# Kernel optimization log

Hardware: AMD Instinct MI355X
Metric: run time of the kernel (lower is better)

## Reference

```python
import jax, jax.numpy as jnp
import numpy as np

C = 512        # channels
CTX = 768      # context_dim


def setup_inputs() -> dict:
    key = jax.random.key(0)
    ks = jax.random.split(key, 10)
    B, H, W = 8, 64, 64
    Lc = 512
    s = 0.02
    return {
        "x": jax.random.normal(ks[0], (B, C, H, W), jnp.float32),
        "context": jax.random.normal(ks[1], (B, Lc, CTX), jnp.float32),
        "Wq": jax.random.normal(ks[2], (C, C), jnp.float32) * s,
        "bq": jnp.zeros((C,), jnp.float32),
        "Wk": jax.random.normal(ks[3], (CTX, C), jnp.float32) * s,
        "bk": jnp.zeros((C,), jnp.float32),
        "Wv": jax.random.normal(ks[4], (CTX, C), jnp.float32) * s,
        "bv": jnp.zeros((C,), jnp.float32),
        "Wo": jax.random.normal(ks[5], (C, C), jnp.float32) * s,
        "bo": jnp.zeros((C,), jnp.float32),
    }


def reference(x, context, Wq, bq, Wk, bk, Wv, bv, Wo, bo):
    B, Cdim, H, W = x.shape
    scale = Cdim ** (-0.5)
    # [B, HW, C]
    xr = x.reshape(B, Cdim, H * W).transpose(0, 2, 1)
    q = xr @ Wq + bq                      # [B, HW, C]
    k = context @ Wk + bk                 # [B, Lc, C]
    v = context @ Wv + bv                 # [B, Lc, C]
    sim = jnp.einsum('bqc,bkc->bqk', q, k) * scale
    attn = jax.nn.softmax(sim, axis=-1)
    out = jnp.einsum('bqk,bkc->bqc', attn, v)
    out = out @ Wo + bo                   # [B, HW, C]
    out = out.transpose(0, 2, 1).reshape(B, Cdim, H, W)
    return x + out
```

## Files before the change

kernel.cpp:

```cpp
#include <hip/hip_runtime.h>
#include <hip/hip_bf16.h>

typedef __bf16 bf16_t;
typedef bf16_t bf16x8 __attribute__((ext_vector_type(8)));
typedef bf16_t bf16x4 __attribute__((ext_vector_type(4)));
typedef float  f32x4  __attribute__((ext_vector_type(4)));

constexpr int B_ = 8, C_ = 512, HW_ = 4096, LC_ = 512, CTX_ = 768;


__global__ void k_transpose_w(const float* __restrict__ in, bf16_t* __restrict__ out,
                              int R, int Cc) {
    __shared__ float t[32][33];
    int r0 = blockIdx.x * 32, c0 = blockIdx.y * 32;
    int tx = threadIdx.x, ty = threadIdx.y;
#pragma unroll
    for (int i = 0; i < 4; ++i)
        t[ty + i * 8][tx] = in[(size_t)(r0 + ty + i * 8) * Cc + c0 + tx];
    __syncthreads();
#pragma unroll
    for (int i = 0; i < 4; ++i)
        out[(size_t)(c0 + ty + i * 8) * R + r0 + tx] = (bf16_t)t[tx][ty + i * 8];
}

__global__ void k_bias(const float* __restrict__ bk, const float* __restrict__ bv,
                       const bf16_t* __restrict__ Wo_t, const float* __restrict__ bo,
                       float* __restrict__ bkvo) {
    int blk = blockIdx.x, tid = threadIdx.x;
    if (blk >= 128) {
        int i = (blk - 128) * 256 + tid;
        bkvo[i] = bk[i];
        return;
    }
    int wave = tid >> 6, lane = tid & 63;
    int cc = blk * 4 + wave;
    bf16x8 w = *(const bf16x8*)&Wo_t[(size_t)cc * C_ + lane * 8];
    float s = 0.f;
#pragma unroll
    for (int j = 0; j < 8; ++j) s += bv[lane * 8 + j] * (float)w[j];
#pragma unroll
    for (int o = 32; o > 0; o >>= 1) s += __shfl_xor(s, o);
    if (lane == 0) bkvo[512 + cc] = s + bo[cc];
}

__global__ void k_f32_to_bf16(const float* __restrict__ in, bf16_t* __restrict__ out, int n) {
    int i = (blockIdx.x * 256 + threadIdx.x) * 4;
    if (i >= n) return;
    f32x4 v = *(const f32x4*)(in + i);
    bf16x4 w;
    w[0] = (bf16_t)v.x; w[1] = (bf16_t)v.y; w[2] = (bf16_t)v.z; w[3] = (bf16_t)v.w;
    *(bf16x4*)(out + i) = w;
}

template <int MODE>
__global__ __launch_bounds__(256) void k_gemm(
    const bf16_t* __restrict__ A, int lda, long sA,
    const bf16_t* __restrict__ Bt, int ldb, long sB,
    const float* __restrict__ bias,
    void* __restrict__ out_, long sOut,
    int N, int K, float scale) {
    __shared__ bf16_t lA[128 * 32];
    __shared__ bf16_t lB[128 * 32];
    const int z = blockIdx.z;
    A  += (size_t)z * sA;
    Bt += (size_t)z * sB;
    const int tid  = threadIdx.x;
    const int lane = tid & 63;
    const int wave = tid >> 6;
    const int wm = (wave >> 1) * 64, wn = (wave & 1) * 64;
    const int bm0 = blockIdx.y * 128, bn0 = blockIdx.x * 128;
    const int ar = lane & 15, kc = lane >> 4;

    auto lA3 = (__attribute__((address_space(3))) char*)&lA[0];
    auto lB3 = (__attribute__((address_space(3))) char*)&lB[0];

    f32x4 acc[4][4] = {};

    for (int k0 = 0; k0 < K; k0 += 32) {
        __syncthreads();
#pragma unroll
        for (int s = 0; s < 2; ++s) {
            int wchunk = wave * 2 + s;
            int id = wchunk * 64 + lane;
            int row = id >> 2, c4 = id & 3;
            __builtin_amdgcn_global_load_lds(
                (const __attribute__((address_space(1))) void*)
                    &A[(size_t)(bm0 + row) * lda + k0 + c4 * 8],
                (__attribute__((address_space(3))) void*)(lA3 + wchunk * 1024),
                16, 0, 0);
            __builtin_amdgcn_global_load_lds(
                (const __attribute__((address_space(1))) void*)
                    &Bt[(size_t)(bn0 + row) * ldb + k0 + c4 * 8],
                (__attribute__((address_space(3))) void*)(lB3 + wchunk * 1024),
                16, 0, 0);
        }
        __syncthreads();
        bf16x8 af[4], bfr[4];
#pragma unroll
        for (int f = 0; f < 4; ++f) {
            af[f]  = *(const bf16x8*)&lA[(wm + f * 16 + ar) * 32 + kc * 8];
            bfr[f] = *(const bf16x8*)&lB[(wn + f * 16 + ar) * 32 + kc * 8];
        }
#pragma unroll
        for (int fm = 0; fm < 4; ++fm)
#pragma unroll
            for (int fn = 0; fn < 4; ++fn)
                acc[fm][fn] = __builtin_amdgcn_mfma_f32_16x16x32_bf16(
                    af[fm], bfr[fn], acc[fm][fn], 0, 0, 0);
    }

    const int rj = (lane >> 4) * 4;
    const int cj = lane & 15;

#pragma unroll
    for (int fm = 0; fm < 4; ++fm) {
#pragma unroll
        for (int fn = 0; fn < 4; ++fn) {
            int r0 = bm0 + wm + fm * 16 + rj;
            int cc = bn0 + wn + fn * 16 + cj;
            if constexpr (MODE == 3) {
                bf16_t* out = (bf16_t*)out_;
                bf16x4 v;
#pragma unroll
                for (int j = 0; j < 4; ++j) v[j] = (bf16_t)acc[fm][fn][j];
                *(bf16x4*)&out[(size_t)cc * sOut + r0] = v;
            } else {
                float bb = bias[cc];
                if (cc < 512) {
                    bf16_t* o = (bf16_t*)out_;
#pragma unroll
                    for (int j = 0; j < 4; ++j)
                        o[(size_t)(r0 + j) * 512 + cc] = (bf16_t)(acc[fm][fn][j] + bb);
                } else {
                    bf16_t* o = (bf16_t*)out_ + (size_t)B_ * LC_ * C_;
                    int b = r0 >> 9, l0 = r0 & 511;
                    bf16x4 v;
#pragma unroll
                    for (int j = 0; j < 4; ++j) v[j] = (bf16_t)(acc[fm][fn][j] + bb);
                    *(bf16x4*)&o[((size_t)b * C_ + (cc - 512)) * LC_ + l0] = v;
                }
            }
        }
    }
}

__global__ __launch_bounds__(512, 2) void k_flash(
    const bf16_t* __restrict__ Wq_t, const float* __restrict__ bq,
    const bf16_t* __restrict__ Kb, const bf16_t* __restrict__ Vt,
    const float* __restrict__ x, float* __restrict__ out) {
    __shared__ bf16_t lQP[64 * 512];
    __shared__ bf16_t lS[3][16384];
    float (*redA)[64] = (float(*)[64])&lQP[0];
    float (*redB)[64] = (float(*)[64])&lQP[512];

    const int bid = blockIdx.x;
    const int z = bid & 7;
    const int q0 = (bid >> 3) * 64;
    const int tid = threadIdx.x;
    const int lane = tid & 63;
    const int wave = tid >> 6;
    const int wm2 = wave >> 2;
    const int wn4 = wave & 3;
    const int h = lane >> 4;
    const int r15 = lane & 15;

    const bf16_t* Kz = Kb + (size_t)z * LC_ * C_;
    const bf16_t* Vz = Vt + (size_t)z * C_ * LC_;
    const float*  xz = x + (size_t)z * C_ * HW_;

    auto lS3 = (__attribute__((address_space(3))) char*)&lS[0][0];

    auto STAGE = [&](int b, const bf16_t* __restrict__ src, int t) {
#pragma unroll
        for (int s = 0; s < 4; ++s) {
            int id = s * 512 + tid;
            int row = id >> 2, c4 = id & 3;
            int c4s = c4 ^ (row & 3);
            __builtin_amdgcn_global_load_lds(
                (const __attribute__((address_space(1))) void*)
                    &src[(size_t)row * 512 + t * 32 + c4s * 8],
                (__attribute__((address_space(3))) void*)
                    (lS3 + b * 32768 + s * 8192 + wave * 1024),
                16, 0, 0);
        }
    };

    f32x4 acc[2][8];
    bf16x8 af0[2], bf0[8], af1[2], bf1[8];

    auto READF = [&](bf16x8 (&af)[2], bf16x8 (&bfr)[8], int t, int buf) {
        int c16 = t * 4 + h;
#pragma unroll
        for (int m = 0; m < 2; ++m) {
            int row = wm2 * 32 + m * 16 + r15;
            int sc = (c16 & 56) | ((c16 ^ row) & 7);
            af[m] = *(const bf16x8*)&lQP[row * 512 + sc * 8];
        }
        const bf16_t* lb = &lS[buf][0];
#pragma unroll
        for (int n = 0; n < 8; ++n) {
            int row = wn4 * 128 + n * 16 + r15;
            bfr[n] = *(const bf16x8*)&lb[row * 32 + (h ^ (row & 3)) * 8];
        }
    };
    auto MF = [&](bf16x8 (&af)[2], bf16x8 (&bfr)[8]) {
        __builtin_amdgcn_s_setprio(1);
#pragma unroll
        for (int m = 0; m < 2; ++m)
#pragma unroll
            for (int n = 0; n < 8; ++n)
                acc[m][n] = __builtin_amdgcn_mfma_f32_16x16x32_bf16(
                    af[m], bfr[n], acc[m][n], 0, 0, 0);
        __builtin_amdgcn_s_setprio(0);
    };
    auto BAR = [&]() {
        __builtin_amdgcn_sched_barrier(0);
        __builtin_amdgcn_s_barrier();
        __builtin_amdgcn_sched_barrier(0);
    };

    auto PHASE = [&](const bf16_t* __restrict__ src, int off) {
        READF(af0, bf0, 0, off % 3);
#pragma unroll
        for (int tt = 0; tt < 7; ++tt) {
            int t = 2 * tt;
            STAGE((t + 2 + off) % 3, src, t + 2);
            MF(af0, bf0);
            asm volatile("s_waitcnt vmcnt(4)" ::: "memory");
            READF(af1, bf1, t + 1, (t + 1 + off) % 3);
            BAR();
            STAGE((t + 3 + off) % 3, src, t + 3);
            MF(af1, bf1);
            asm volatile("s_waitcnt vmcnt(4)" ::: "memory");
            READF(af0, bf0, t + 2, (t + 2 + off) % 3);
            BAR();
        }
        MF(af0, bf0);
        asm volatile("s_waitcnt vmcnt(0)" ::: "memory");
        READF(af1, bf1, 15, (15 + off) % 3);
        BAR();
        MF(af1, bf1);
    };

    STAGE(0, Wq_t, 0); STAGE(1, Wq_t, 1);
#pragma unroll
    for (int i = 0; i < 16; ++i) {
        int c = i * 32 + (tid >> 4);
        int q = (tid & 15) * 4;
        f32x4 v = *(const f32x4*)&xz[(size_t)c * HW_ + q0 + q];
#pragma unroll
        for (int j = 0; j < 4; ++j) {
            int row = q + j;
            int c16 = c >> 3;
            int sc = (c16 & 56) | ((c16 ^ row) & 7);
            lQP[row * 512 + sc * 8 + (c & 7)] = (bf16_t)v[j];
        }
    }
    __syncthreads();

#pragma unroll
    for (int m = 0; m < 2; ++m)
#pragma unroll
        for (int n = 0; n < 8; ++n) acc[m][n] = (f32x4)0.f;
    PHASE(Wq_t, 0);

    __syncthreads();
    STAGE(1, Kz, 0); STAGE(2, Kz, 1);
    {
        float bqv[8];
#pragma unroll
        for (int n = 0; n < 8; ++n) bqv[n] = bq[wn4 * 128 + n * 16 + r15];
#pragma unroll
        for (int m = 0; m < 2; ++m)
#pragma unroll
            for (int j = 0; j < 4; ++j) {
                int row = wm2 * 32 + m * 16 + h * 4 + j;
#pragma unroll
                for (int n = 0; n < 8; ++n) {
                    int col = wn4 * 128 + n * 16 + r15;
                    int c16 = col >> 3;
                    int sc = (c16 & 56) | ((c16 ^ row) & 7);
                    lQP[row * 512 + sc * 8 + (col & 7)] = (bf16_t)(acc[m][n][j] + bqv[n]);
                }
            }
    }
    __syncthreads();

#pragma unroll
    for (int m = 0; m < 2; ++m)
#pragma unroll
        for (int n = 0; n < 8; ++n) acc[m][n] = (f32x4)0.f;
    PHASE(Kz, 1);

    __syncthreads();
    STAGE(2, Vz, 0); STAGE(0, Vz, 1);
    const float scale = 0.044194173824159216f;
    float M[2][4], inv[2][4];
#pragma unroll
    for (int m = 0; m < 2; ++m)
#pragma unroll
        for (int j = 0; j < 4; ++j) {
            float v = -1e30f;
#pragma unroll
            for (int n = 0; n < 8; ++n) v = fmaxf(v, acc[m][n][j]);
#pragma unroll
            for (int o = 1; o < 16; o <<= 1) v = fmaxf(v, __shfl_xor(v, o));
            if (r15 == 0) redA[wn4][wm2 * 32 + m * 16 + h * 4 + j] = v;
        }
    __syncthreads();
#pragma unroll
    for (int m = 0; m < 2; ++m)
#pragma unroll
        for (int j = 0; j < 4; ++j) {
            int row = wm2 * 32 + m * 16 + h * 4 + j;
            M[m][j] = fmaxf(fmaxf(redA[0][row], redA[1][row]),
                            fmaxf(redA[2][row], redA[3][row]));
        }
#pragma unroll
    for (int m = 0; m < 2; ++m)
#pragma unroll
        for (int j = 0; j < 4; ++j) {
            float s = 0.f;
#pragma unroll
            for (int n = 0; n < 8; ++n) {
                float e = __expf((acc[m][n][j] - M[m][j]) * scale);
                acc[m][n][j] = e;
                s += e;
            }
#pragma unroll
            for (int o = 1; o < 16; o <<= 1) s += __shfl_xor(s, o);
            if (r15 == 0) redB[wn4][wm2 * 32 + m * 16 + h * 4 + j] = s;
        }
    __syncthreads();
#pragma unroll
    for (int m = 0; m < 2; ++m)
#pragma unroll
        for (int j = 0; j < 4; ++j) {
            int row = wm2 * 32 + m * 16 + h * 4 + j;
            inv[m][j] = 1.f / (redB[0][row] + redB[1][row] +
                               redB[2][row] + redB[3][row]);
        }
    __syncthreads();
#pragma unroll
    for (int m = 0; m < 2; ++m)
#pragma unroll
        for (int j = 0; j < 4; ++j) {
            int row = wm2 * 32 + m * 16 + h * 4 + j;
#pragma unroll
            for (int n = 0; n < 8; ++n) {
                int col = wn4 * 128 + n * 16 + r15;
                int c16 = col >> 3;
                int sc = (c16 & 56) | ((c16 ^ row) & 7);
                lQP[row * 512 + sc * 8 + (col & 7)] = (bf16_t)(acc[m][n][j] * inv[m][j]);
            }
        }
    __syncthreads();

#pragma unroll
    for (int m = 0; m < 2; ++m)
#pragma unroll
        for (int n = 0; n < 8; ++n) acc[m][n] = (f32x4)0.f;
    PHASE(Vz, 2);

    float* oz = out + (size_t)z * C_ * HW_;
#pragma unroll
    for (int m = 0; m < 2; ++m)
#pragma unroll
        for (int n = 0; n < 8; ++n) {
            int r0 = q0 + wm2 * 32 + m * 16 + h * 4;
            int cc = wn4 * 128 + n * 16 + r15;
            f32x4 xv = *(const f32x4*)&xz[(size_t)cc * HW_ + r0];
            f32x4 o;
#pragma unroll
            for (int j = 0; j < 4; ++j) o[j] = acc[m][n][j] + xv[j];
            *(f32x4*)&oz[(size_t)cc * HW_ + r0] = o;
        }
}

extern "C" void kernel_launch(void* const* d_in, const int* in_sizes, int n_in,
                              void* d_out, int out_size, void* d_ws, size_t ws_size,
                              hipStream_t stream) {
    (void)in_sizes; (void)n_in; (void)out_size; (void)ws_size;
    const float* x   = (const float*)d_in[0];
    const float* ctx = (const float*)d_in[1];
    const float* Wq  = (const float*)d_in[2];
    const float* bq  = (const float*)d_in[3];
    const float* Wk  = (const float*)d_in[4];
    const float* bk  = (const float*)d_in[5];
    const float* Wv  = (const float*)d_in[6];
    const float* bv  = (const float*)d_in[7];
    const float* Wo  = (const float*)d_in[8];
    const float* bo  = (const float*)d_in[9];
    float* out = (float*)d_out;

    char* ws = (char*)d_ws;
    size_t off = 0;
    auto alloc = [&](size_t bytes) {
        char* p = ws + off;
        off += (bytes + 255) & ~(size_t)255;
        return p;
    };
    bf16_t* Wq_t  = (bf16_t*)alloc((size_t)C_ * C_ * 2);
    bf16_t* Wk_t  = (bf16_t*)alloc((size_t)C_ * CTX_ * 2);
    bf16_t* Wvo_t = (bf16_t*)alloc((size_t)C_ * CTX_ * 2);
    bf16_t* Wv_b  = (bf16_t*)alloc((size_t)CTX_ * C_ * 2);
    bf16_t* Wo_t  = (bf16_t*)alloc((size_t)C_ * C_ * 2);
    float*  bkvo  = (float*)alloc((size_t)1024 * 4);
    bf16_t* ctxb  = (bf16_t*)alloc((size_t)B_ * LC_ * CTX_ * 2);
    bf16_t* Kb    = (bf16_t*)alloc((size_t)B_ * LC_ * C_ * 2);
    bf16_t* Vt    = (bf16_t*)alloc((size_t)B_ * C_ * LC_ * 2);

    k_transpose_w<<<dim3(C_ / 32, C_ / 32), dim3(32, 8), 0, stream>>>(Wq, Wq_t, C_, C_);
    k_transpose_w<<<dim3(CTX_ / 32, C_ / 32), dim3(32, 8), 0, stream>>>(Wk, Wk_t, CTX_, C_);
    k_transpose_w<<<dim3(C_ / 32, C_ / 32), dim3(32, 8), 0, stream>>>(Wo, Wo_t, C_, C_);
    k_f32_to_bf16<<<(CTX_ * C_ / 4 + 255) / 256, 256, 0, stream>>>(Wv, Wv_b, CTX_ * C_);
    k_bias<<<130, 256, 0, stream>>>(bk, bv, Wo_t, bo, bkvo);
    k_f32_to_bf16<<<(B_ * LC_ * CTX_ / 4 + 255) / 256, 256, 0, stream>>>(
        ctx, ctxb, B_ * LC_ * CTX_);

    k_gemm<3><<<dim3(4, 6, 1), 256, 0, stream>>>(
        Wv_b, C_, 0, Wo_t, C_, 0, nullptr, Wvo_t, CTX_, C_, C_, 1.f);
    k_gemm<4><<<dim3(8, 32, 1), 256, 0, stream>>>(
        ctxb, CTX_, 0, Wk_t, CTX_, 0, bkvo, Kb, 0, 1024, CTX_, 1.f);
    k_flash<<<512, 512, 0, stream>>>(Wq_t, bq, Kb, Vt, x, out);
}
```

Before: 165.6 us.

## Change LDS swizzles, simplify flash pipeline loop, merge weight transposes

Changes the LDS swizzle for the Q/P tile (adds row>>3 into the XOR) and for the staged K/V/W tiles (uses row>>1) to reduce bank conflicts on the fragment reads. It replaces the double-buffered register prefetch in the phase loop with a simpler per-iteration load-then-compute loop, which lowers register pressure but exposes LDS read latency. It also merges three weight-transpose launches into one kernel using blockIdx.z, and moves redB to avoid overlap with redA.

Measured after the change: 188.6 us. +13.8%, slower.

```diff
diff --git a/kernel.cpp b/kernel.cpp
--- a/kernel.cpp
+++ b/kernel.cpp
@@ -9,14 +9,21 @@
 constexpr int B_ = 8, C_ = 512, HW_ = 4096, LC_ = 512, CTX_ = 768;
 
 
-__global__ void k_transpose_w(const float* __restrict__ in, bf16_t* __restrict__ out,
-                              int R, int Cc) {
+__global__ void k_transpose_w3(const float* __restrict__ Wq, const float* __restrict__ Wk,
+                               const float* __restrict__ Wo,
+                               bf16_t* __restrict__ Wq_t, bf16_t* __restrict__ Wk_t,
+                               bf16_t* __restrict__ Wo_t) {
     __shared__ float t[32][33];
+    int zz = blockIdx.z;
+    const float* in = (zz == 0) ? Wq : (zz == 1) ? Wk : Wo;
+    bf16_t* out     = (zz == 0) ? Wq_t : (zz == 1) ? Wk_t : Wo_t;
+    int R = (zz == 1) ? CTX_ : C_;
     int r0 = blockIdx.x * 32, c0 = blockIdx.y * 32;
+    if (r0 >= R) return;
     int tx = threadIdx.x, ty = threadIdx.y;
 #pragma unroll
     for (int i = 0; i < 4; ++i)
-        t[ty + i * 8][tx] = in[(size_t)(r0 + ty + i * 8) * Cc + c0 + tx];
+        t[ty + i * 8][tx] = in[(size_t)(r0 + ty + i * 8) * C_ + c0 + tx];
     __syncthreads();
 #pragma unroll
     for (int i = 0; i < 4; ++i)
@@ -144,6 +151,7 @@
     }
 }
 
+#define SWZ(c16, row) ((((c16)) & 56) | (((c16) ^ (row) ^ ((row) >> 3)) & 7))
 __global__ __launch_bounds__(512, 2) void k_flash(
     const bf16_t* __restrict__ Wq_t, const float* __restrict__ bq,
     const bf16_t* __restrict__ Kb, const bf16_t* __restrict__ Vt,
@@ -151,7 +159,7 @@
     __shared__ bf16_t lQP[64 * 512];
     __shared__ bf16_t lS[3][16384];
     float (*redA)[64] = (float(*)[64])&lQP[0];
-    float (*redB)[64] = (float(*)[64])&lQP[512];
+    float (*redB)[64] = (float(*)[64])&lQP[1024];
 
     const int bid = blockIdx.x;
     const int z = bid & 7;
@@ -175,7 +183,7 @@
         for (int s = 0; s < 4; ++s) {
             int id = s * 512 + tid;
             int row = id >> 2, c4 = id & 3;
-            int c4s = c4 ^ (row & 3);
+            int c4s = c4 ^ ((row >> 1) & 3);
             __builtin_amdgcn_global_load_lds(
                 (const __attribute__((address_space(1))) void*)
                     &src[(size_t)row * 512 + t * 32 + c4s * 8],
@@ -186,60 +194,39 @@
     };
 
     f32x4 acc[2][8];
-    bf16x8 af0[2], bf0[8], af1[2], bf1[8];
-
-    auto READF = [&](bf16x8 (&af)[2], bf16x8 (&bfr)[8], int t, int buf) {
-        int c16 = t * 4 + h;
-#pragma unroll
-        for (int m = 0; m < 2; ++m) {
-            int row = wm2 * 32 + m * 16 + r15;
-            int sc = (c16 & 56) | ((c16 ^ row) & 7);
-            af[m] = *(const bf16x8*)&lQP[row * 512 + sc * 8];
-        }
-        const bf16_t* lb = &lS[buf][0];
-#pragma unroll
-        for (int n = 0; n < 8; ++n) {
-            int row = wn4 * 128 + n * 16 + r15;
-            bfr[n] = *(const bf16x8*)&lb[row * 32 + (h ^ (row & 3)) * 8];
-        }
-    };
-    auto MF = [&](bf16x8 (&af)[2], bf16x8 (&bfr)[8]) {
-        __builtin_amdgcn_s_setprio(1);
-#pragma unroll
-        for (int m = 0; m < 2; ++m)
-#pragma unroll
-            for (int n = 0; n < 8; ++n)
-                acc[m][n] = __builtin_amdgcn_mfma_f32_16x16x32_bf16(
-                    af[m], bfr[n], acc[m][n], 0, 0, 0);
-        __builtin_amdgcn_s_setprio(0);
-    };
-    auto BAR = [&]() {
-        __builtin_amdgcn_sched_barrier(0);
-        __builtin_amdgcn_s_barrier();
-        __builtin_amdgcn_sched_barrier(0);
-    };
 
     auto PHASE = [&](const bf16_t* __restrict__ src, int off) {
-        READF(af0, bf0, 0, off % 3);
-#pragma unroll
-        for (int tt = 0; tt < 7; ++tt) {
-            int t = 2 * tt;
-            STAGE((t + 2 + off) % 3, src, t + 2);
-            MF(af0, bf0);
-            asm volatile("s_waitcnt vmcnt(4)" ::: "memory");
-            READF(af1, bf1, t + 1, (t + 1 + off) % 3);
-            BAR();
-            STAGE((t + 3 + off) % 3, src, t + 3);
-            MF(af1, bf1);
-            asm volatile("s_waitcnt vmcnt(4)" ::: "memory");
-            READF(af0, bf0, t + 2, (t + 2 + off) % 3);
-            BAR();
-        }
-        MF(af0, bf0);
-        asm volatile("s_waitcnt vmcnt(0)" ::: "memory");
-        READF(af1, bf1, 15, (15 + off) % 3);
-        BAR();
-        MF(af1, bf1);
+        for (int t = 0; t < 16; ++t) {
+            if (t <= 13) STAGE((t + 2 + off) % 3, src, t + 2);
+            bf16x8 af[2], bfr[8];
+            int c16 = t * 4 + h;
+#pragma unroll
+            for (int m = 0; m < 2; ++m) {
+                int row = wm2 * 32 + m * 16 + r15;
+                af[m] = *(const bf16x8*)&lQP[row * 512 + SWZ(c16, row) * 8];
+            }
+            const bf16_t* lb = &lS[(t + off) % 3][0];
+#pragma unroll
+            for (int n = 0; n < 8; ++n) {
+                int row = wn4 * 128 + n * 16 + r15;
+                bfr[n] = *(const bf16x8*)&lb[row * 32 + ((h ^ (row >> 1)) & 3) * 8];
+            }
+            __builtin_amdgcn_s_setprio(1);
+#pragma unroll
+            for (int m = 0; m < 2; ++m)
+#pragma unroll
+                for (int n = 0; n < 8; ++n)
+                    acc[m][n] = __builtin_amdgcn_mfma_f32_16x16x32_bf16(
+                        af[m], bfr[n], acc[m][n], 0, 0, 0);
+            __builtin_amdgcn_s_setprio(0);
+            if (t < 15) {
+                if (t <= 13) asm volatile("s_waitcnt vmcnt(4)" ::: "memory");
+                else         asm volatile("s_waitcnt vmcnt(0)" ::: "memory");
+                __builtin_amdgcn_sched_barrier(0);
+                __builtin_amdgcn_s_barrier();
+                __builtin_amdgcn_sched_barrier(0);
+            }
+        }
     };
 
     STAGE(0, Wq_t, 0); STAGE(1, Wq_t, 1);
@@ -248,12 +235,11 @@
         int c = i * 32 + (tid >> 4);
         int q = (tid & 15) * 4;
         f32x4 v = *(const f32x4*)&xz[(size_t)c * HW_ + q0 + q];
+        int c16 = c >> 3;
 #pragma unroll
         for (int j = 0; j < 4; ++j) {
             int row = q + j;
-            int c16 = c >> 3;
-            int sc = (c16 & 56) | ((c16 ^ row) & 7);
-            lQP[row * 512 + sc * 8 + (c & 7)] = (bf16_t)v[j];
+            lQP[row * 512 + SWZ(c16, row) * 8 + (c & 7)] = (bf16_t)v[j];
         }
     }
     __syncthreads();
@@ -279,8 +265,8 @@
                 for (int n = 0; n < 8; ++n) {
                     int col = wn4 * 128 + n * 16 + r15;
                     int c16 = col >> 3;
-                    int sc = (c16 & 56) | ((c16 ^ row) & 7);
-                    lQP[row * 512 + sc * 8 + (col & 7)] = (bf16_t)(acc[m][n][j] + bqv[n]);
+                    lQP[row * 512 + SWZ(c16, row) * 8 + (col & 7)] =
+                        (bf16_t)(acc[m][n][j] + bqv[n]);
                 }
             }
     }
@@ -350,8 +336,8 @@
             for (int n = 0; n < 8; ++n) {
                 int col = wn4 * 128 + n * 16 + r15;
                 int c16 = col >> 3;
-                int sc = (c16 & 56) | ((c16 ^ row) & 7);
-                lQP[row * 512 + sc * 8 + (col & 7)] = (bf16_t)(acc[m][n][j] * inv[m][j]);
+                lQP[row * 512 + SWZ(c16, row) * 8 + (col & 7)] =
+                    (bf16_t)(acc[m][n][j] * inv[m][j]);
             }
         }
     __syncthreads();
@@ -410,9 +396,8 @@
     bf16_t* Kb    = (bf16_t*)alloc((size_t)B_ * LC_ * C_ * 2);
     bf16_t* Vt    = (bf16_t*)alloc((size_t)B_ * C_ * LC_ * 2);
 
-    k_transpose_w<<<dim3(C_ / 32, C_ / 32), dim3(32, 8), 0, stream>>>(Wq, Wq_t, C_, C_);
-    k_transpose_w<<<dim3(CTX_ / 32, C_ / 32), dim3(32, 8), 0, stream>>>(Wk, Wk_t, CTX_, C_);
-    k_transpose_w<<<dim3(C_ / 32, C_ / 32), dim3(32, 8), 0, stream>>>(Wo, Wo_t, C_, C_);
+    k_transpose_w3<<<dim3(CTX_ / 32, C_ / 32, 3), dim3(32, 8), 0, stream>>>(
+        Wq, Wk, Wo, Wq_t, Wk_t, Wo_t);
     k_f32_to_bf16<<<(CTX_ * C_ / 4 + 255) / 256, 256, 0, stream>>>(Wv, Wv_b, CTX_ * C_);
     k_bias<<<130, 256, 0, stream>>>(bk, bv, Wo_t, bo, bkvo);
     k_f32_to_bf16<<<(B_ * LC_ * CTX_ / 4 + 255) / 256, 256, 0, stream>>>(
```
